# Kernel tuning notes

Measured on AMD Instinct MI355X. Metric: run time of the kernel, lower is better.

## Reference

```python
import jax, jax.numpy as jnp
import numpy as np

D_MODEL = 1024
NUM_HEADS = 16


def setup_inputs() -> dict:
    key = jax.random.key(0)
    ks = jax.random.split(key, 11)
    B, L, D = 1, 4096, D_MODEL
    s = 1.0 / np.sqrt(D)
    inp = {
        "Q": jax.random.normal(ks[0], (B, L, D), jnp.float32),
        "K": jax.random.normal(ks[1], (B, L, D), jnp.float32),
        "V": jax.random.normal(ks[2], (B, L, D), jnp.float32),
        "w_q": jax.random.normal(ks[3], (D, D), jnp.float32) * s,
        "b_q": jax.random.normal(ks[4], (D,), jnp.float32) * s,
        "w_k": jax.random.normal(ks[5], (D, D), jnp.float32) * s,
        "b_k": jax.random.normal(ks[6], (D,), jnp.float32) * s,
        "w_v": jax.random.normal(ks[7], (D, D), jnp.float32) * s,
        "b_v": jax.random.normal(ks[8], (D,), jnp.float32) * s,
        "w_o": jax.random.normal(ks[9], (D, D), jnp.float32) * s,
        "b_o": jax.random.normal(ks[10], (D,), jnp.float32) * s,
    }
    return inp


def _split_heads(x, n_heads):
    B, L, D = x.shape
    return x.reshape(B, L, n_heads, D // n_heads).transpose(0, 2, 1, 3)  # (B,H,L,Dh)


def reference(Q, K, V, w_q, b_q, w_k, b_k, w_v, b_v, w_o, b_o):
    H = NUM_HEADS
    # QKV projections (torch Linear: x @ W.T + b)
    q = _split_heads(Q @ w_q.T + b_q, H)
    k = _split_heads(K @ w_k.T + b_k, H)
    v = _split_heads(V @ w_v.T + b_v, H)
    d_h = q.shape[-1]
    scores = jnp.einsum("bhqd,bhkd->bhqk", q, k) / jnp.sqrt(jnp.float32(d_h))
    attn = jax.nn.softmax(scores, axis=-1)
    out = jnp.einsum("bhqk,bhkd->bhqd", attn, v)  # (B,H,L,Dh)
    B, _, L, _ = out.shape
    out = out.transpose(0, 2, 1, 3).reshape(B, L, H * d_h)
    return out @ w_o.T + b_o
```

## Files before the change

kernel.cpp:

```cpp
#include <hip/hip_runtime.h>
#include <hip/hip_bf16.h>
#include <stdint.h>

#define D_MODEL 1024
#define NHEAD   16
#define DH      64

typedef __attribute__((ext_vector_type(8))) short bf16x8;
typedef __attribute__((ext_vector_type(4))) float f32x4;

__device__ __forceinline__ ushort f2bf(float f) {
    __hip_bfloat16 h = __float2bfloat16(f);
    return *reinterpret_cast<ushort*>(&h);
}

__device__ __forceinline__ void gload_lds16(const void* g, void* l) {
    __builtin_amdgcn_global_load_lds(
        (const __attribute__((address_space(1))) void*)g,
        (__attribute__((address_space(3))) void*)l, 16, 0, 0);
}

__device__ __forceinline__ bf16x8 load8f(const float* p) {
    const float4 a = *(const float4*)p;
    const float4 b = *(const float4*)(p + 4);
    bf16x8 r;
    r[0] = (short)f2bf(a.x); r[1] = (short)f2bf(a.y);
    r[2] = (short)f2bf(a.z); r[3] = (short)f2bf(a.w);
    r[4] = (short)f2bf(b.x); r[5] = (short)f2bf(b.y);
    r[6] = (short)f2bf(b.z); r[7] = (short)f2bf(b.w);
    return r;
}

__global__ __launch_bounds__(256) void cvt_w_kernel(
    const float* __restrict__ w0, const float* __restrict__ w1,
    const float* __restrict__ w2, const float* __restrict__ w3,
    ushort* __restrict__ out)
{
    const int g = blockIdx.x * 256 + threadIdx.x;
    const int m = g >> 17;
    const int off = (g & 131071) * 8;
    const float* src = (m == 0) ? w0 : (m == 1) ? w1 : (m == 2) ? w2 : w3;
    *(bf16x8*)(out + (size_t)m * 1048576 + off) = load8f(src + off);
}

__global__ __launch_bounds__(256) void cvt_all_kernel(
    const float* __restrict__ w0, const float* __restrict__ w1,
    const float* __restrict__ w2, const float* __restrict__ w3,
    const float* __restrict__ X0, const float* __restrict__ X1,
    const float* __restrict__ X2,
    ushort* __restrict__ Wb,
    ushort* __restrict__ Qb, ushort* __restrict__ Kb, ushort* __restrict__ Vb,
    int igrp)
{
    const int g = blockIdx.x * 256 + threadIdx.x;
    if (g < 524288) {
        const int m = g >> 17;
        const int off = (g & 131071) * 8;
        const float* src = (m == 0) ? w0 : (m == 1) ? w1 : (m == 2) ? w2 : w3;
        *(bf16x8*)(Wb + (size_t)m * 1048576 + off) = load8f(src + off);
    } else {
        const int g2 = g - 524288;
        if (g2 >= 3 * igrp) return;
        const int m = g2 / igrp;
        const int off = (g2 - m * igrp) * 8;
        const float* src = (m == 0) ? X0 : (m == 1) ? X1 : X2;
        ushort* dst = (m == 0) ? Qb : (m == 1) ? Kb : Vb;
        *(bf16x8*)(dst + off) = load8f(src + off);
    }
}

__device__ __forceinline__ void storeC(float*  C, size_t i, float v) { C[i] = v; }
__device__ __forceinline__ void storeC(ushort* C, size_t i, float v) { C[i] = (short)f2bf(v); }

__device__ __forceinline__ void xcd_swizzle(int& bx, int& by) {
    if (gridDim.x == 8 && (gridDim.y & 7) == 0) {
        const int fid   = by * 8 + bx;
        const int xcd   = fid & 7;
        const int local = fid >> 3;
        const int rpx   = gridDim.y >> 3;
        by = xcd * rpx + (local >> 3);
        bx = local & 7;
    }
}

template<int NW, bool A_F32, typename TX, typename TOUT>
__device__ __forceinline__ void gemm_core(
    const TX* __restrict__ X,
    const ushort* __restrict__ Wb,
    const float* __restrict__ Bias,
    TOUT* __restrict__ C,
    int M, int N, int K, float scale,
    int bx, int by,
    short* As, short* Bs)
{
    const int tid  = threadIdx.x;
    const int w    = tid >> 6;
    const int lane = tid & 63;
    const int quad = lane >> 4;
    const int l15  = lane & 15;
    const int wr   = (NW == 4) ? (w >> 1) : (w >> 2);
    const int wc   = (NW == 4) ? (w & 1)  : (w & 3);
    const int NJ   = (NW == 4) ? 4 : 2;
    const int colw = (NW == 4) ? 64 : 32;

    const int m0 = by * 128;
    const int n0 = bx * 128;

    f32x4 acc[4][4] = {};

    for (int k0 = 0; k0 < K; k0 += 32) {
        __syncthreads();
        #pragma unroll
        for (int c = 0; c < 8 / NW; ++c) {
            int chunk = w * (8 / NW) + c;
            int row   = chunk * 16 + (lane >> 2);
            gload_lds16(Wb + (size_t)(n0 + row) * K + k0 + (lane & 3) * 8,
                        &Bs[chunk * 512]);
        }
        if constexpr (A_F32) {
            #pragma unroll
            for (int c = 0; c < 2; ++c) {
                int idx = c * 256 + tid;
                int row = idx >> 2;
                int col = (idx & 3) * 8;
                *(bf16x8*)&As[row * 32 + col] =
                    load8f((const float*)X + (size_t)(m0 + row) * K + k0 + col);
            }
        } else {
            #pragma unroll
            for (int c = 0; c < 8 / NW; ++c) {
                int chunk = w * (8 / NW) + c;
                int row   = chunk * 16 + (lane >> 2);
                gload_lds16((const ushort*)X + (size_t)(m0 + row) * K + k0 + (lane & 3) * 8,
                            &As[chunk * 512]);
            }
        }
        __syncthreads();

        bf16x8 af[4], bfr[4];
        #pragma unroll
        for (int i = 0; i < 4; ++i)
            af[i] = *(const bf16x8*)&As[(wr * 64 + i * 16 + l15) * 32 + quad * 8];
        #pragma unroll
        for (int j = 0; j < NJ; ++j)
            bfr[j] = *(const bf16x8*)&Bs[(wc * colw + j * 16 + l15) * 32 + quad * 8];
        #pragma unroll
        for (int i = 0; i < 4; ++i)
            #pragma unroll
            for (int j = 0; j < NJ; ++j)
                acc[i][j] = __builtin_amdgcn_mfma_f32_16x16x32_bf16(af[i], bfr[j], acc[i][j], 0, 0, 0);
    }

    float bias[4];
    #pragma unroll
    for (int j = 0; j < NJ; ++j)
        bias[j] = Bias[n0 + wc * colw + j * 16 + l15];

    #pragma unroll
    for (int i = 0; i < 4; ++i) {
        int row = m0 + wr * 64 + i * 16 + quad * 4;
        #pragma unroll
        for (int j = 0; j < NJ; ++j) {
            int col = n0 + wc * colw + j * 16 + l15;
            #pragma unroll
            for (int r = 0; r < 4; ++r)
                storeC(C, (size_t)(row + r) * N + col, (acc[i][j][r] + bias[j]) * scale);
        }
    }
}

__global__ __launch_bounds__(256) void qkv_proj_f32_kernel(
    const float* __restrict__ Qin, const float* __restrict__ Kin,
    const float* __restrict__ Vin,
    const ushort* __restrict__ Wb,
    const float* __restrict__ Bq, const float* __restrict__ Bk,
    const float* __restrict__ Bv,
    ushort* qo, ushort* ko, ushort* vo, int L)
{
    __shared__ short As[4096];
    __shared__ short Bs[4096];
    const int z = blockIdx.z;
    const float *X, *B; ushort* C;
    float scale = 1.0f;
    if (z == 0)      { X = Qin; B = Bq; C = qo; scale = 0.125f * 1.44269504088896f; }
    else if (z == 1) { X = Kin; B = Bk; C = ko; }
    else             { X = Vin; B = Bv; C = vo; }
    int bx = blockIdx.x, by = blockIdx.y;
    xcd_swizzle(bx, by);
    gemm_core<4, true, float, ushort>(X, Wb + (size_t)z * 1048576, B, C,
                                      L, D_MODEL, D_MODEL, scale, bx, by, As, Bs);
}

__global__ __launch_bounds__(256) void qkv_proj_bf16_kernel(
    const ushort* __restrict__ Qb, const ushort* __restrict__ Kb,
    const ushort* __restrict__ Vb,
    const ushort* __restrict__ Wb,
    const float* __restrict__ Bq, const float* __restrict__ Bk,
    const float* __restrict__ Bv,
    ushort* qo, ushort* ko, ushort* vo, int L)
{
    __shared__ short As[4096];
    __shared__ short Bs[4096];

    const int gy    = gridDim.y;
    const int slice = gy * 8;
    const int total = slice * 3;
    const int phys  = (blockIdx.z * gy + blockIdx.y) * 8 + blockIdx.x;
    int lz, lx, ly;
    if ((total & 7) == 0) {
        const int logical = (phys & 7) * (total >> 3) + (phys >> 3);
        lz = logical / slice;
        const int lrem = logical - lz * slice;
        ly = lrem >> 3;
        lx = lrem & 7;
    } else {
        lz = blockIdx.z; ly = blockIdx.y; lx = blockIdx.x;
    }

    const ushort *X; const float* B; ushort* C;
    float scale = 1.0f;
    if (lz == 0)      { X = Qb; B = Bq; C = qo; scale = 0.125f * 1.44269504088896f; }
    else if (lz == 1) { X = Kb; B = Bk; C = ko; }
    else              { X = Vb; B = Bv; C = vo; }
    gemm_core<4, false, ushort, ushort>(X, Wb + (size_t)lz * 1048576, B, C,
                                        L, D_MODEL, D_MODEL, scale, lx, ly, As, Bs);
}

__global__ __launch_bounds__(512) void out_proj_kernel(
    const ushort* __restrict__ Xa, const ushort* __restrict__ Wb,
    const float* __restrict__ Bo, float* out, int L)
{
    __shared__ short As[4096];
    __shared__ short Bs[4096];
    int bx = blockIdx.x, by = blockIdx.y;
    xcd_swizzle(bx, by);
    gemm_core<8, false, ushort, float>(Xa, Wb + (size_t)3 * 1048576, Bo, out,
                                       L, D_MODEL, D_MODEL, 1.0f, bx, by, As, Bs);
}

__global__ __launch_bounds__(512) void attn_kernel(
    const ushort* __restrict__ Qw,
    const ushort* __restrict__ Kw,
    const ushort* __restrict__ Vw,
    ushort* __restrict__ Ow, int L)
{
    __shared__ short Ks[64 * 64];
    __shared__ short Vs[64 * 64];
    __shared__ short Ps[8][16 * 64];

    const int tid  = threadIdx.x;
    const int w    = tid >> 6;
    const int lane = tid & 63;
    const int quad = lane >> 4;
    const int l15  = lane & 15;
    const int h    = blockIdx.y;
    const int q0   = blockIdx.x * 128;

    const ushort* qp = Qw + (size_t)(q0 + w * 16 + l15) * D_MODEL + h * DH + quad * 8;
    bf16x8 qf0 = *(const bf16x8*)(qp);
    bf16x8 qf1 = *(const bf16x8*)(qp + 32);

    const int kkey = tid >> 3;
    const int kc8  = tid & 7;
    const int vkey = lane;
    const int vdh  = w * 8;

    const int krswz0 = ((quad    ) ^ (l15 & 7)) * 8;
    const int krswz1 = ((quad + 4) ^ (l15 & 7)) * 8;

    f32x4 o[4] = {};
    float l_run = 0.f;

    const ushort* kptr = Kw + (size_t)kkey * D_MODEL + h * DH + kc8 * 8;
    const ushort* vptr = Vw + (size_t)vkey * D_MODEL + h * DH + vdh;
    bf16x8 kreg = *(const bf16x8*)kptr;
    bf16x8 vreg = *(const bf16x8*)vptr;

    for (int key0 = 0; key0 < L; key0 += 64) {
        __syncthreads();
        *(bf16x8*)&Ks[kkey * 64 + ((kc8 ^ (kkey & 7)) * 8)] = kreg;
        #pragma unroll
        for (int i = 0; i < 8; ++i)
            Vs[(vdh + i) * 64 + (((vkey >> 3) ^ i) * 8) + (vkey & 7)] = vreg[i];
        __syncthreads();

        if (key0 + 64 < L) {
            kptr += (size_t)64 * D_MODEL;
            vptr += (size_t)64 * D_MODEL;
            kreg = *(const bf16x8*)kptr;
            vreg = *(const bf16x8*)vptr;
        }

        f32x4 st[4];
        __builtin_amdgcn_s_setprio(1);
        #pragma unroll
        for (int kt = 0; kt < 4; ++kt) {
            const int kr = (kt * 16 + l15) * 64;
            bf16x8 kf0 = *(const bf16x8*)&Ks[kr + krswz0];
            bf16x8 kf1 = *(const bf16x8*)&Ks[kr + krswz1];
            f32x4 z = {};
            z = __builtin_amdgcn_mfma_f32_16x16x32_bf16(kf0, qf0, z, 0, 0, 0);
            z = __builtin_amdgcn_mfma_f32_16x16x32_bf16(kf1, qf1, z, 0, 0, 0);
            st[kt] = z;
        }
        __builtin_amdgcn_s_setprio(0);

        float rs = 0.f;
        #pragma unroll
        for (int kt = 0; kt < 4; ++kt) {
            float p0 = __builtin_amdgcn_exp2f(st[kt][0]);
            float p1 = __builtin_amdgcn_exp2f(st[kt][1]);
            float p2 = __builtin_amdgcn_exp2f(st[kt][2]);
            float p3 = __builtin_amdgcn_exp2f(st[kt][3]);
            rs += (p0 + p1) + (p2 + p3);
            uint2 pk;
            pk.x = (uint32_t)f2bf(p0) | ((uint32_t)f2bf(p1) << 16);
            pk.y = (uint32_t)f2bf(p2) | ((uint32_t)f2bf(p3) << 16);
            const int G = kt * 2 + (quad >> 1);
            *(uint2*)&Ps[w][l15 * 64 + ((G ^ (l15 & 7)) * 8) + (quad & 1) * 4] = pk;
        }
        l_run += rs;

        __builtin_amdgcn_s_setprio(1);
        #pragma unroll
        for (int f = 0; f < 2; ++f) {
            bf16x8 pf = *(const bf16x8*)&Ps[w][l15 * 64 + (((f * 4 + quad) ^ (l15 & 7)) * 8)];
            #pragma unroll
            for (int dt = 0; dt < 4; ++dt) {
                bf16x8 vf = *(const bf16x8*)&Vs[(dt * 16 + l15) * 64 + (((f * 4 + quad) ^ (l15 & 7)) * 8)];
                o[dt] = __builtin_amdgcn_mfma_f32_16x16x32_bf16(pf, vf, o[dt], 0, 0, 0);
            }
        }
        __builtin_amdgcn_s_setprio(0);
    }

    l_run += __shfl_xor(l_run, 16);
    l_run += __shfl_xor(l_run, 32);
    const float inv = 1.f / l_run;
    #pragma unroll
    for (int r = 0; r < 4; ++r) {
        const float linv = __shfl(inv, (lane & 48) | (quad * 4 + r));
        const int row = q0 + w * 16 + quad * 4 + r;
        #pragma unroll
        for (int dt = 0; dt < 4; ++dt) {
            int col = h * DH + dt * 16 + l15;
            Ow[(size_t)row * D_MODEL + col] = (short)f2bf(o[dt][r] * linv);
        }
    }
}

extern "C" void kernel_launch(void* const* d_in, const int* in_sizes, int n_in,
                              void* d_out, int out_size, void* d_ws, size_t ws_size,
                              hipStream_t stream) {
    const float* Q   = (const float*)d_in[0];
    const float* K   = (const float*)d_in[1];
    const float* V   = (const float*)d_in[2];
    const float* w_q = (const float*)d_in[3];
    const float* b_q = (const float*)d_in[4];
    const float* w_k = (const float*)d_in[5];
    const float* b_k = (const float*)d_in[6];
    const float* w_v = (const float*)d_in[7];
    const float* b_v = (const float*)d_in[8];
    const float* w_o = (const float*)d_in[9];
    const float* b_o = (const float*)d_in[10];
    float* out = (float*)d_out;

    const int L = in_sizes[0] / D_MODEL;
    const size_t mat = (size_t)L * D_MODEL;

    ushort* Wb   = (ushort*)d_ws;
    ushort* q_ws = (ushort*)d_out;
    ushort* k_ws = q_ws + mat;
    const bool ext = ws_size >= (size_t)40 * 1024 * 1024;

    ushort *a_ws, *v_ws, *Qb = nullptr, *Kb = nullptr, *Vb = nullptr;
    if (ext) {
        Vb   = (ushort*)d_ws + 4 * 1048576;
        v_ws = Vb + mat;
        Qb   = v_ws + mat;
        Kb   = Qb + mat;
        a_ws = Vb;
    } else {
        a_ws = (ushort*)d_ws + 4 * 1048576;
        v_ws = a_ws + mat;
    }

    if (ext) {
        const int igrp = (int)(mat / 8);
        const int total = 524288 + 3 * igrp;
        cvt_all_kernel<<<dim3((total + 255) / 256), dim3(256), 0, stream>>>(
            w_q, w_k, w_v, w_o, Q, K, V, Wb, Qb, Kb, Vb, igrp);
        dim3 gqkv(D_MODEL / 128, L / 128, 3);
        qkv_proj_bf16_kernel<<<gqkv, dim3(256), 0, stream>>>(Qb, Kb, Vb, Wb,
                                                             b_q, b_k, b_v,
                                                             q_ws, k_ws, v_ws, L);
    } else {
        cvt_w_kernel<<<dim3(2048), dim3(256), 0, stream>>>(w_q, w_k, w_v, w_o, Wb);
        dim3 gqkv(D_MODEL / 128, L / 128, 3);
        qkv_proj_f32_kernel<<<gqkv, dim3(256), 0, stream>>>(Q, K, V, Wb,
                                                            b_q, b_k, b_v,
                                                            q_ws, k_ws, v_ws, L);
    }
    dim3 gattn(L / 128, NHEAD);
    attn_kernel<<<gattn, dim3(512), 0, stream>>>(q_ws, k_ws, v_ws, a_ws, L);
    dim3 gout(D_MODEL / 128, L / 128);
    out_proj_kernel<<<gout, dim3(512), 0, stream>>>(a_ws, Wb, b_o, out, L);
}
```

Baseline: 264.2 us.

## Prefetch two K/V tiles ahead and remap attention blocks for cache locality

The attention loop now keeps two register-staged K/V tiles in flight, loading each tile two iterations ahead, so global-load latency has more compute to hide behind. Block indices are also remapped from a linear id so that consecutive blocks spread across heads in a chosen order, which is meant to improve L2/MALL sharing of K/V across concurrently running blocks. It costs extra registers for the second prefetch buffer and assumes NT is even, with a fixed 32×16 grid layout.

```diff
diff --git a/kernel.cpp b/kernel.cpp
--- a/kernel.cpp
+++ b/kernel.cpp
@@ -253,8 +253,11 @@
     const int lane = tid & 63;
     const int quad = lane >> 4;
     const int l15  = lane & 15;
-    const int h    = blockIdx.y;
-    const int q0   = blockIdx.x * 128;
+
+    const int p   = blockIdx.y * gridDim.x + blockIdx.x;
+    const int slot = p >> 3;
+    const int h   = (p & 7) * 2 + (slot >> 5);
+    const int q0  = (slot & 31) * 128;
 
     const ushort* qp = Qw + (size_t)(q0 + w * 16 + l15) * D_MODEL + h * DH + quad * 8;
     bf16x8 qf0 = *(const bf16x8*)(qp);
@@ -268,29 +271,23 @@
     const int krswz0 = ((quad    ) ^ (l15 & 7)) * 8;
     const int krswz1 = ((quad + 4) ^ (l15 & 7)) * 8;
 
+    const int kwofs = kkey * 64 + ((kc8 ^ (kkey & 7)) * 8);
+
     f32x4 o[4] = {};
     float l_run = 0.f;
 
-    const ushort* kptr = Kw + (size_t)kkey * D_MODEL + h * DH + kc8 * 8;
-    const ushort* vptr = Vw + (size_t)vkey * D_MODEL + h * DH + vdh;
-    bf16x8 kreg = *(const bf16x8*)kptr;
-    bf16x8 vreg = *(const bf16x8*)vptr;
-
-    for (int key0 = 0; key0 < L; key0 += 64) {
-        __syncthreads();
-        *(bf16x8*)&Ks[kkey * 64 + ((kc8 ^ (kkey & 7)) * 8)] = kreg;
-        #pragma unroll
-        for (int i = 0; i < 8; ++i)
-            Vs[(vdh + i) * 64 + (((vkey >> 3) ^ i) * 8) + (vkey & 7)] = vreg[i];
-        __syncthreads();
-
-        if (key0 + 64 < L) {
-            kptr += (size_t)64 * D_MODEL;
-            vptr += (size_t)64 * D_MODEL;
-            kreg = *(const bf16x8*)kptr;
-            vreg = *(const bf16x8*)vptr;
-        }
-
+    const size_t dstep = (size_t)64 * D_MODEL;
+    const ushort* kp = Kw + (size_t)kkey * D_MODEL + h * DH + kc8 * 8;
+    const ushort* vp = Vw + (size_t)vkey * D_MODEL + h * DH + vdh;
+
+    bf16x8 k0 = *(const bf16x8*)kp;
+    bf16x8 v0 = *(const bf16x8*)vp;
+    bf16x8 k1 = *(const bf16x8*)(kp + dstep);
+    bf16x8 v1 = *(const bf16x8*)(vp + dstep);
+
+    const int NT = L >> 6;
+
+    auto compute = [&]() {
         f32x4 st[4];
         __builtin_amdgcn_s_setprio(1);
         #pragma unroll
@@ -332,6 +329,34 @@
             }
         }
         __builtin_amdgcn_s_setprio(0);
+    };
+
+    for (int t = 0; t < NT; t += 2) {
+        __syncthreads();
+        *(bf16x8*)&Ks[kwofs] = k0;
+        #pragma unroll
+        for (int i = 0; i < 8; ++i)
+            Vs[(vdh + i) * 64 + (((vkey >> 3) ^ i) * 8) + (vkey & 7)] = v0[i];
+        __syncthreads();
+        if (t + 2 < NT) {
+            kp += 2 * dstep;
+            vp += 2 * dstep;
+            k0 = *(const bf16x8*)kp;
+            v0 = *(const bf16x8*)vp;
+        }
+        compute();
+
+        __syncthreads();
+        *(bf16x8*)&Ks[kwofs] = k1;
+        #pragma unroll
+        for (int i = 0; i < 8; ++i)
+            Vs[(vdh + i) * 64 + (((vkey >> 3) ^ i) * 8) + (vkey & 7)] = v1[i];
+        __syncthreads();
+        if (t + 3 < NT) {
+            k1 = *(const bf16x8*)(kp + dstep);
+            v1 = *(const bf16x8*)(vp + dstep);
+        }
+        compute();
     }
 
     l_run += __shfl_xor(l_run, 16);
```

Result: no change. 263.9 us (median of 2 runs) (-0.1%).

## Have each attention wave process two query tiles to reuse K/V fragments

Applied to the files above, without the earlier changes.

The attention kernel drops from 512 to 256 threads per block, and each wave now handles 32 query rows as two 16-row tiles. K and V fragments are loaded from LDS once and reused for both tiles, halving LDS reads per MFMA. Blocks are also remapped so consecutive blocks land on different heads/XCDs, which should improve L2 locality for K/V. The cost is more registers per thread (two accumulator sets, cached fragments), which may lower occupancy. The code also hardcodes 32 query tiles (L=4096) in the block index remap.

```diff
diff --git a/kernel.cpp b/kernel.cpp
--- a/kernel.cpp
+++ b/kernel.cpp
@@ -238,7 +238,7 @@
                                        L, D_MODEL, D_MODEL, 1.0f, bx, by, As, Bs);
 }
 
-__global__ __launch_bounds__(512) void attn_kernel(
+__global__ __launch_bounds__(256) void attn_kernel(
     const ushort* __restrict__ Qw,
     const ushort* __restrict__ Kw,
     const ushort* __restrict__ Vw,
@@ -246,105 +246,177 @@
 {
     __shared__ short Ks[64 * 64];
     __shared__ short Vs[64 * 64];
-    __shared__ short Ps[8][16 * 64];
+    __shared__ short Ps[4][16 * 64];
 
     const int tid  = threadIdx.x;
     const int w    = tid >> 6;
     const int lane = tid & 63;
     const int quad = lane >> 4;
     const int l15  = lane & 15;
-    const int h    = blockIdx.y;
-    const int q0   = blockIdx.x * 128;
-
-    const ushort* qp = Qw + (size_t)(q0 + w * 16 + l15) * D_MODEL + h * DH + quad * 8;
-    bf16x8 qf0 = *(const bf16x8*)(qp);
-    bf16x8 qf1 = *(const bf16x8*)(qp + 32);
-
-    const int kkey = tid >> 3;
-    const int kc8  = tid & 7;
-    const int vkey = lane;
-    const int vdh  = w * 8;
+
+    const int p    = blockIdx.y * gridDim.x + blockIdx.x;
+    const int slot = p >> 3;
+    const int h    = (p & 7) * 2 + (slot >> 5);
+    const int q0   = (slot & 31) * 128;
+
+    const ushort* qpA = Qw + (size_t)(q0 + w * 32 + l15) * D_MODEL + h * DH + quad * 8;
+    const ushort* qpB = qpA + (size_t)16 * D_MODEL;
+    bf16x8 qA0 = *(const bf16x8*)(qpA);
+    bf16x8 qA1 = *(const bf16x8*)(qpA + 32);
+    bf16x8 qB0 = *(const bf16x8*)(qpB);
+    bf16x8 qB1 = *(const bf16x8*)(qpB + 32);
+
+    const int kkey = tid >> 2;
+    const int kc   = tid & 3;
+    const int vkey = tid & 63;
+    const int vg   = tid >> 6;
+    const int kw0  = kkey * 64 + ((kc ^ (kkey & 7)) * 8);
+    const int kw1  = kkey * 64 + (((kc + 4) ^ (kkey & 7)) * 8);
 
     const int krswz0 = ((quad    ) ^ (l15 & 7)) * 8;
     const int krswz1 = ((quad + 4) ^ (l15 & 7)) * 8;
 
-    f32x4 o[4] = {};
-    float l_run = 0.f;
-
-    const ushort* kptr = Kw + (size_t)kkey * D_MODEL + h * DH + kc8 * 8;
-    const ushort* vptr = Vw + (size_t)vkey * D_MODEL + h * DH + vdh;
-    bf16x8 kreg = *(const bf16x8*)kptr;
-    bf16x8 vreg = *(const bf16x8*)vptr;
+    f32x4 oA[4] = {}, oB[4] = {};
+    float lA = 0.f, lB = 0.f;
+
+    const size_t dstep = (size_t)64 * D_MODEL;
+    const ushort* kp = Kw + (size_t)kkey * D_MODEL + h * DH + kc * 8;
+    const ushort* vp = Vw + (size_t)vkey * D_MODEL + h * DH + vg * 16;
+
+    bf16x8 kr0 = *(const bf16x8*)kp;
+    bf16x8 kr1 = *(const bf16x8*)(kp + 32);
+    bf16x8 vr0 = *(const bf16x8*)vp;
+    bf16x8 vr1 = *(const bf16x8*)(vp + 8);
 
     for (int key0 = 0; key0 < L; key0 += 64) {
         __syncthreads();
-        *(bf16x8*)&Ks[kkey * 64 + ((kc8 ^ (kkey & 7)) * 8)] = kreg;
-        #pragma unroll
-        for (int i = 0; i < 8; ++i)
-            Vs[(vdh + i) * 64 + (((vkey >> 3) ^ i) * 8) + (vkey & 7)] = vreg[i];
+        *(bf16x8*)&Ks[kw0] = kr0;
+        *(bf16x8*)&Ks[kw1] = kr1;
+        #pragma unroll
+        for (int i = 0; i < 8; ++i) {
+            const int d0 = vg * 16 + i;
+            const int d1 = d0 + 8;
+            Vs[d0 * 64 + (((vkey >> 3) ^ (d0 & 7)) * 8) + (vkey & 7)] = vr0[i];
+            Vs[d1 * 64 + (((vkey >> 3) ^ (d1 & 7)) * 8) + (vkey & 7)] = vr1[i];
+        }
         __syncthreads();
 
         if (key0 + 64 < L) {
-            kptr += (size_t)64 * D_MODEL;
-            vptr += (size_t)64 * D_MODEL;
-            kreg = *(const bf16x8*)kptr;
-            vreg = *(const bf16x8*)vptr;
-        }
-
-        f32x4 st[4];
-        __builtin_amdgcn_s_setprio(1);
+            kp += dstep; vp += dstep;
+            kr0 = *(const bf16x8*)kp;
+            kr1 = *(const bf16x8*)(kp + 32);
+            vr0 = *(const bf16x8*)vp;
+            vr1 = *(const bf16x8*)(vp + 8);
+        }
+
+        bf16x8 kf[8];
         #pragma unroll
         for (int kt = 0; kt < 4; ++kt) {
             const int kr = (kt * 16 + l15) * 64;
-            bf16x8 kf0 = *(const bf16x8*)&Ks[kr + krswz0];
-            bf16x8 kf1 = *(const bf16x8*)&Ks[kr + krswz1];
+            kf[2 * kt]     = *(const bf16x8*)&Ks[kr + krswz0];
+            kf[2 * kt + 1] = *(const bf16x8*)&Ks[kr + krswz1];
+        }
+
+        f32x4 stA[4], stB[4];
+        __builtin_amdgcn_s_setprio(1);
+        #pragma unroll
+        for (int kt = 0; kt < 4; ++kt) {
             f32x4 z = {};
-            z = __builtin_amdgcn_mfma_f32_16x16x32_bf16(kf0, qf0, z, 0, 0, 0);
-            z = __builtin_amdgcn_mfma_f32_16x16x32_bf16(kf1, qf1, z, 0, 0, 0);
-            st[kt] = z;
+            z = __builtin_amdgcn_mfma_f32_16x16x32_bf16(kf[2 * kt], qA0, z, 0, 0, 0);
+            z = __builtin_amdgcn_mfma_f32_16x16x32_bf16(kf[2 * kt + 1], qA1, z, 0, 0, 0);
+            stA[kt] = z;
+        }
+        #pragma unroll
+        for (int kt = 0; kt < 4; ++kt) {
+            f32x4 z = {};
+            z = __builtin_amdgcn_mfma_f32_16x16x32_bf16(kf[2 * kt], qB0, z, 0, 0, 0);
+            z = __builtin_amdgcn_mfma_f32_16x16x32_bf16(kf[2 * kt + 1], qB1, z, 0, 0, 0);
+            stB[kt] = z;
         }
         __builtin_amdgcn_s_setprio(0);
 
-        float rs = 0.f;
-        #pragma unroll
-        for (int kt = 0; kt < 4; ++kt) {
-            float p0 = __builtin_amdgcn_exp2f(st[kt][0]);
-            float p1 = __builtin_amdgcn_exp2f(st[kt][1]);
-            float p2 = __builtin_amdgcn_exp2f(st[kt][2]);
-            float p3 = __builtin_amdgcn_exp2f(st[kt][3]);
-            rs += (p0 + p1) + (p2 + p3);
-            uint2 pk;
-            pk.x = (uint32_t)f2bf(p0) | ((uint32_t)f2bf(p1) << 16);
-            pk.y = (uint32_t)f2bf(p2) | ((uint32_t)f2bf(p3) << 16);
-            const int G = kt * 2 + (quad >> 1);
-            *(uint2*)&Ps[w][l15 * 64 + ((G ^ (l15 & 7)) * 8) + (quad & 1) * 4] = pk;
-        }
-        l_run += rs;
-
-        __builtin_amdgcn_s_setprio(1);
-        #pragma unroll
-        for (int f = 0; f < 2; ++f) {
-            bf16x8 pf = *(const bf16x8*)&Ps[w][l15 * 64 + (((f * 4 + quad) ^ (l15 & 7)) * 8)];
-            #pragma unroll
-            for (int dt = 0; dt < 4; ++dt) {
-                bf16x8 vf = *(const bf16x8*)&Vs[(dt * 16 + l15) * 64 + (((f * 4 + quad) ^ (l15 & 7)) * 8)];
-                o[dt] = __builtin_amdgcn_mfma_f32_16x16x32_bf16(pf, vf, o[dt], 0, 0, 0);
-            }
-        }
-        __builtin_amdgcn_s_setprio(0);
-    }
-
-    l_run += __shfl_xor(l_run, 16);
-    l_run += __shfl_xor(l_run, 32);
-    const float inv = 1.f / l_run;
+        bf16x8 vf[8];
+        #pragma unroll
+        for (int f = 0; f < 2; ++f)
+            #pragma unroll
+            for (int dt = 0; dt < 4; ++dt)
+                vf[f * 4 + dt] = *(const bf16x8*)&Vs[(dt * 16 + l15) * 64 +
+                                                     (((f * 4 + quad) ^ (l15 & 7)) * 8)];
+
+        {
+            float rs = 0.f;
+            #pragma unroll
+            for (int kt = 0; kt < 4; ++kt) {
+                float p0 = __builtin_amdgcn_exp2f(stA[kt][0]);
+                float p1 = __builtin_amdgcn_exp2f(stA[kt][1]);
+                float p2 = __builtin_amdgcn_exp2f(stA[kt][2]);
+                float p3 = __builtin_amdgcn_exp2f(stA[kt][3]);
+                rs += (p0 + p1) + (p2 + p3);
+                uint2 pk;
+                pk.x = (uint32_t)f2bf(p0) | ((uint32_t)f2bf(p1) << 16);
+                pk.y = (uint32_t)f2bf(p2) | ((uint32_t)f2bf(p3) << 16);
+                const int G = kt * 2 + (quad >> 1);
+                *(uint2*)&Ps[w][l15 * 64 + ((G ^ (l15 & 7)) * 8) + (quad & 1) * 4] = pk;
+            }
+            lA += rs;
+
+            __builtin_amdgcn_s_setprio(1);
+            #pragma unroll
+            for (int f = 0; f < 2; ++f) {
+                bf16x8 pf = *(const bf16x8*)&Ps[w][l15 * 64 + (((f * 4 + quad) ^ (l15 & 7)) * 8)];
+                #pragma unroll
+                for (int dt = 0; dt < 4; ++dt)
+                    oA[dt] = __builtin_amdgcn_mfma_f32_16x16x32_bf16(pf, vf[f * 4 + dt], oA[dt], 0, 0, 0);
+            }
+            __builtin_amdgcn_s_setprio(0);
+        }
+
+        {
+            float rs = 0.f;
+            #pragma unroll
+            for (int kt = 0; kt < 4; ++kt) {
+                float p0 = __builtin_amdgcn_exp2f(stB[kt][0]);
+                float p1 = __builtin_amdgcn_exp2f(stB[kt][1]);
+                float p2 = __builtin_amdgcn_exp2f(stB[kt][2]);
+                float p3 = __builtin_amdgcn_exp2f(stB[kt][3]);
+                rs += (p0 + p1) + (p2 + p3);
+                uint2 pk;
+                pk.x = (uint32_t)f2bf(p0) | ((uint32_t)f2bf(p1) << 16);
+                pk.y = (uint32_t)f2bf(p2) | ((uint32_t)f2bf(p3) << 16);
+                const int G = kt * 2 + (quad >> 1);
+                *(uint2*)&Ps[w][l15 * 64 + ((G ^ (l15 & 7)) * 8) + (quad & 1) * 4] = pk;
+            }
+            lB += rs;
+
+            __builtin_amdgcn_s_setprio(1);
+            #pragma unroll
+            for (int f = 0; f < 2; ++f) {
+                bf16x8 pf = *(const bf16x8*)&Ps[w][l15 * 64 + (((f * 4 + quad) ^ (l15 & 7)) * 8)];
+                #pragma unroll
+                for (int dt = 0; dt < 4; ++dt)
+                    oB[dt] = __builtin_amdgcn_mfma_f32_16x16x32_bf16(pf, vf[f * 4 + dt], oB[dt], 0, 0, 0);
+            }
+            __builtin_amdgcn_s_setprio(0);
+        }
+    }
+
+    lA += __shfl_xor(lA, 16);
+    lA += __shfl_xor(lA, 32);
+    lB += __shfl_xor(lB, 16);
+    lB += __shfl_xor(lB, 32);
+    const float invA = 1.f / lA;
+    const float invB = 1.f / lB;
     #pragma unroll
     for (int r = 0; r < 4; ++r) {
-        const float linv = __shfl(inv, (lane & 48) | (quad * 4 + r));
-        const int row = q0 + w * 16 + quad * 4 + r;
+        const float liA = __shfl(invA, (lane & 48) | (quad * 4 + r));
+        const float liB = __shfl(invB, (lane & 48) | (quad * 4 + r));
+        const int rowA = q0 + w * 32 + quad * 4 + r;
+        const int rowB = rowA + 16;
         #pragma unroll
         for (int dt = 0; dt < 4; ++dt) {
             int col = h * DH + dt * 16 + l15;
-            Ow[(size_t)row * D_MODEL + col] = (short)f2bf(o[dt][r] * linv);
+            Ow[(size_t)rowA * D_MODEL + col] = (short)f2bf(oA[dt][r] * liA);
+            Ow[(size_t)rowB * D_MODEL + col] = (short)f2bf(oB[dt][r] * liB);
         }
     }
 }
@@ -402,7 +474,7 @@
                                                             q_ws, k_ws, v_ws, L);
     }
     dim3 gattn(L / 128, NHEAD);
-    attn_kernel<<<gattn, dim3(512), 0, stream>>>(q_ws, k_ws, v_ws, a_ws, L);
+    attn_kernel<<<gattn, dim3(256), 0, stream>>>(q_ws, k_ws, v_ws, a_ws, L);
     dim3 gout(D_MODEL / 128, L / 128);
     out_proj_kernel<<<gout, dim3(512), 0, stream>>>(a_ws, Wb, b_o, out, L);
 }
```

Result: slower. 271.8 us (+2.9%).
